# Optimization experiments

Measured on AMD Instinct MI355X. Metric: run time of the kernel, lower is better.

Reference implementation:

```python
import jax, jax.numpy as jnp
import numpy as np

N_NODES = 10000
N_EDGES = 640000
F_IN = 128
HID = 128
N_LAYERS = 3
N_ACT = 4096
NEG_SLOPE = 0.2


def setup_inputs() -> dict:
    key = jax.random.key(0)
    ks = jax.random.split(key, 16)
    s = 0.05
    return {
        "x": jax.random.normal(ks[0], (N_NODES, F_IN), jnp.float32),
        "edge_index": jax.random.randint(ks[1], (2, N_EDGES), 0, N_NODES, jnp.int64),
        "action_src": jax.random.randint(ks[2], (N_ACT,), 0, N_NODES, jnp.int64),
        "action_dst": jax.random.randint(ks[3], (N_ACT,), 0, N_NODES, jnp.int64),
        "action_type": jax.random.randint(ks[4], (N_ACT,), 0, 2, jnp.int32),
        "gat_W": jax.random.normal(ks[5], (N_LAYERS, HID, HID), jnp.float32) * s,
        "gat_asrc": jax.random.normal(ks[6], (N_LAYERS, HID), jnp.float32) * s,
        "gat_adst": jax.random.normal(ks[7], (N_LAYERS, HID), jnp.float32) * s,
        "gat_b": jax.random.normal(ks[8], (N_LAYERS, HID), jnp.float32) * s,
        "mlp_W1": jax.random.normal(ks[9], (2 * HID + 1, HID), jnp.float32) * s,
        "mlp_b1": jax.random.normal(ks[10], (HID,), jnp.float32) * s,
        "mlp_W2": jax.random.normal(ks[11], (HID, 1), jnp.float32) * s,
        "mlp_b2": jax.random.normal(ks[12], (1,), jnp.float32) * s,
    }


def _gat_layer(h, src, dst, W, a_src, a_dst, b, n_nodes):
    # PyG GATConv, heads=1: z = h W; e_ij = leaky_relu(a_src.z_j + a_dst.z_i)
    z = h @ W                                   # [N, HID]
    e = jax.nn.leaky_relu((z @ a_src)[src] + (z @ a_dst)[dst], NEG_SLOPE)  # [E+N]
    m = jax.ops.segment_max(e, dst, num_segments=n_nodes)
    m = jnp.where(jnp.isfinite(m), m, 0.0)
    ex = jnp.exp(e - m[dst])
    denom = jax.ops.segment_sum(ex, dst, num_segments=n_nodes)
    alpha = ex / denom[dst]                     # softmax over incoming edges
    out = jax.ops.segment_sum(alpha[:, None] * z[src], dst, num_segments=n_nodes)
    return out + b


def reference(x, edge_index, action_src, action_dst, action_type,
              gat_W, gat_asrc, gat_adst, gat_b,
              mlp_W1, mlp_b1, mlp_W2, mlp_b2):
    n = x.shape[0]
    loop = jnp.arange(n, dtype=edge_index.dtype)  # add_self_loops=True
    src = jnp.concatenate([edge_index[0], loop])
    dst = jnp.concatenate([edge_index[1], loop])
    h = x
    for l in range(N_LAYERS):
        h = jax.nn.relu(_gat_layer(h, src, dst, gat_W[l], gat_asrc[l], gat_adst[l], gat_b[l], n))
    # vectorized action scoring: [h[src], h[dst], type_flag] -> MLP -> scalar
    feat = jnp.concatenate(
        [h[action_src], h[action_dst], action_type.astype(h.dtype)[:, None]], axis=-1)
    hidden = jax.nn.relu(feat @ mlp_W1 + mlp_b1)
    scores = (hidden @ mlp_W2 + mlp_b2)[:, 0]   # [N_ACT]
    return scores
```

## Files before the change

kernel.cpp:

```cpp
#include <hip/hip_runtime.h>
#include <hip/hip_bf16.h>
#include <hip/hip_fp16.h>

#define N_NODES 10000
#define N_EDGES 640000
#define TOT_E   (N_EDGES + N_NODES)
#define HID     128
#define NEG_SLOPE 0.2f
#define N_ACT   4096

#define NBKT   250
#define NPB    40
#define P1_EPB 4096
#define P1_EPT 16
#define P1_BLOCKS 159
#define SLOTP  56

__global__ __launch_bounds__(256) void part1_k(const int* __restrict__ ei,
                                               unsigned* __restrict__ bpart,
                                               int* __restrict__ bcnt) {
    __shared__ int hist[256];
    __shared__ int lofs[256];
    __shared__ int sc[256];
    __shared__ unsigned stage[P1_EPB];
    __shared__ unsigned char bkt_of[P1_EPB];
    int t = threadIdx.x;
    hist[t] = 0;
    __syncthreads();

    unsigned pk[P1_EPT];
    int bk[P1_EPT];
    int e0 = blockIdx.x * P1_EPB;
#pragma unroll
    for (int i = 0; i < P1_EPT; i++) {
        int e = e0 + i * 256 + t;
        if (e < TOT_E) {
            int src, dst;
            if (e < N_EDGES) { src = ei[e]; dst = ei[N_EDGES + e]; }
            else             { src = e - N_EDGES; dst = src; }
            pk[i] = ((unsigned)dst << 16) | (unsigned)src;
            bk[i] = dst / NPB;
            atomicAdd(&hist[bk[i]], 1);
        } else bk[i] = -1;
    }
    __syncthreads();
    int v = hist[t];
    sc[t] = v;
    __syncthreads();
    for (int o = 1; o < 256; o <<= 1) {
        int u = (t >= o) ? sc[t - o] : 0;
        __syncthreads();
        sc[t] += u;
        __syncthreads();
    }
    lofs[t] = sc[t] - v;
    bcnt[blockIdx.x * 256 + t] = v;
    hist[t] = 0;
    __syncthreads();
#pragma unroll
    for (int i = 0; i < P1_EPT; i++) {
        if (bk[i] >= 0) {
            int p = atomicAdd(&hist[bk[i]], 1);
            int slot = lofs[bk[i]] + p;
            stage[slot] = pk[i];
            bkt_of[slot] = (unsigned char)bk[i];
        }
    }
    __syncthreads();
    int nv = min(P1_EPB, TOT_E - e0);
    for (int s = t; s < nv; s += 256) {
        int b = bkt_of[s];
        bpart[b * (P1_BLOCKS * SLOTP) + blockIdx.x * SLOTP + (s - lofs[b])] = stage[s];
    }
}

__global__ __launch_bounds__(256) void part2_k(const unsigned* __restrict__ bpart,
                                               const int* __restrict__ bcnt,
                                               int* __restrict__ csr,
                                               int* __restrict__ offs) {
    __shared__ unsigned ebuf[4096];
    __shared__ int sc[256];
    __shared__ int nhist[NPB];
    __shared__ int bstart_s, cnt_s;
    int b = blockIdx.x, t = threadIdx.x;

    int tot = 0;
    if (t < NBKT)
        for (int blk = 0; blk < P1_BLOCKS; blk++) tot += bcnt[blk * 256 + t];
    sc[t] = (t < NBKT) ? tot : 0;
    __syncthreads();
    for (int o = 1; o < 256; o <<= 1) {
        int u = (t >= o) ? sc[t - o] : 0;
        __syncthreads();
        sc[t] += u;
        __syncthreads();
    }
    if (t == b) { bstart_s = sc[t] - tot; cnt_s = tot; }
    if (b == 0 && t == 255) offs[N_NODES] = sc[255];
    __syncthreads();

    int L = (t < P1_BLOCKS) ? bcnt[t * 256 + b] : 0;
    sc[t] = L;
    __syncthreads();
    for (int o = 1; o < 256; o <<= 1) {
        int u = (t >= o) ? sc[t - o] : 0;
        __syncthreads();
        sc[t] += u;
        __syncthreads();
    }
    int P = sc[t] - L;
    if (t < NPB) nhist[t] = 0;
    if (t < P1_BLOCKS && L > 0) {
        const unsigned* myrun = bpart + b * (P1_BLOCKS * SLOTP) + t * SLOTP;
        for (int i = 0; i < L; i++) ebuf[P + i] = myrun[i];
    }
    __syncthreads();

    int cnt = cnt_s;
    int n0 = b * NPB;
    for (int i = t; i < cnt; i += 256) atomicAdd(&nhist[(ebuf[i] >> 16) - n0], 1);
    __syncthreads();
    if (t < 64) {
        int v2 = (t < NPB) ? nhist[t] : 0;
        int s2 = v2;
        for (int o = 1; o < 64; o <<= 1) {
            int u = __shfl_up(s2, o, 64);
            if (t >= o) s2 += u;
        }
        if (t < NPB) {
            int ofs = bstart_s + s2 - v2;
            nhist[t] = ofs;
            offs[n0 + t] = ofs;
        }
    }
    __syncthreads();
    for (int i = t; i < cnt; i += 256) {
        unsigned pk = ebuf[i];
        int p = atomicAdd(&nhist[(pk >> 16) - n0], 1);
        csr[p] = pk & 0xFFFF;
    }
}

__device__ __forceinline__ void agg_node(const __half2* __restrict__ z2,
                                         const float* __restrict__ zsi, float zdn,
                                         const int* __restrict__ csr, int o0, int deg,
                                         int lane, float& accx, float& accy, float& denom) {
    for (int base = 0; base < deg; base += 64) {
        int j = base + lane;
        int sreg = 0;
        float ex = 0.f;
        if (j < deg) {
            int s = csr[o0 + j];
            sreg = s;
            float e = zsi[s] + zdn;
            e = e > 0.f ? e : NEG_SLOPE * e;
            ex = __expf(e);
        }
        int cnt = min(64, deg - base);
        int q = 0;
        for (; q + 8 <= cnt; q += 8) {
#pragma unroll
            for (int u = 0; u < 8; u++) {
                int sq = __builtin_amdgcn_readlane(sreg, q + u);
                float exq = __uint_as_float(
                    __builtin_amdgcn_readlane(__float_as_uint(ex), q + u));
                denom += exq;
                float2 vf = __half22float2(z2[sq * 64]);
                accx = fmaf(exq, vf.x, accx);
                accy = fmaf(exq, vf.y, accy);
            }
        }
        for (; q < cnt; q++) {
            int sq = __builtin_amdgcn_readlane(sreg, q);
            float exq = __uint_as_float(
                __builtin_amdgcn_readlane(__float_as_uint(ex), q));
            denom += exq;
            float2 vf = __half22float2(z2[sq * 64]);
            accx = fmaf(exq, vf.x, accx);
            accy = fmaf(exq, vf.y, accy);
        }
    }
}

__device__ __forceinline__ void gload_lds16(const float* g, float* l) {
    __builtin_amdgcn_global_load_lds(
        (const __attribute__((address_space(1))) void*)g,
        (__attribute__((address_space(3))) void*)l, 16, 0, 0);
}

__global__ __launch_bounds__(256) void gemm_k(const float* __restrict__ A,
                                              const float* __restrict__ W,
                                              const float* __restrict__ avs,
                                              const float* __restrict__ avd,
                                              __half* __restrict__ z16,
                                              float* __restrict__ zs,
                                              float* __restrict__ zd) {
    __shared__ float As[32 * HID];
    __shared__ float Ws[HID * HID];
    int t = threadIdx.x;
    int w = t >> 6, lane = t & 63;
    int row0 = blockIdx.x * 32;

#pragma unroll
    for (int i = 0; i < 4; i++) {
        int chunk = w * 4 + i;
        long foff = (long)row0 * HID + chunk * 256;
        const float* g = ((foff + 256) <= (long)N_NODES * HID) ? (A + foff + lane * 4)
                                                               : (A + lane * 4);
        gload_lds16(g, As + chunk * 256);
    }
#pragma unroll
    for (int i = 0; i < 16; i++) {
        int chunk = w * 16 + i;
        gload_lds16(W + chunk * 256 + lane * 4, Ws + chunk * 256);
    }
    __syncthreads();

    int tx = t & 31, ty = t >> 5;
    int r0 = ty * 4;
    float acc[4][4] = {{0.f}};
#pragma unroll 4
    for (int k4 = 0; k4 < 32; k4++) {
        float ak[4][4];
#pragma unroll
        for (int r = 0; r < 4; r++) {
            float4 a4 = *(const float4*)&As[(r0 + r) * HID + k4 * 4];
            ak[r][0] = a4.x; ak[r][1] = a4.y; ak[r][2] = a4.z; ak[r][3] = a4.w;
        }
        const float* Wb = &Ws[k4 * 4 * HID + tx * 4];
#pragma unroll
        for (int kk = 0; kk < 4; kk++) {
            float4 wv = *(const float4*)&Wb[kk * HID];
#pragma unroll
            for (int r = 0; r < 4; r++) {
                acc[r][0] = fmaf(ak[r][kk], wv.x, acc[r][0]);
                acc[r][1] = fmaf(ak[r][kk], wv.y, acc[r][1]);
                acc[r][2] = fmaf(ak[r][kk], wv.z, acc[r][2]);
                acc[r][3] = fmaf(ak[r][kk], wv.w, acc[r][3]);
            }
        }
    }
    float4 asv = *(const float4*)&avs[tx * 4];
    float4 adv = *(const float4*)&avd[tx * 4];
#pragma unroll
    for (int r = 0; r < 4; r++) {
        int row = row0 + r0 + r;
        if (row < N_NODES) {
            *(__half2*)&z16[row * HID + tx * 4]     = __floats2half2_rn(acc[r][0], acc[r][1]);
            *(__half2*)&z16[row * HID + tx * 4 + 2] = __floats2half2_rn(acc[r][2], acc[r][3]);
        }
        float ps = acc[r][0] * asv.x + acc[r][1] * asv.y + acc[r][2] * asv.z + acc[r][3] * asv.w;
        float pd = acc[r][0] * adv.x + acc[r][1] * adv.y + acc[r][2] * adv.z + acc[r][3] * adv.w;
#pragma unroll
        for (int o = 1; o < 32; o <<= 1) {
            ps += __shfl_xor(ps, o, 64);
            pd += __shfl_xor(pd, o, 64);
        }
        if (tx == 0 && row < N_NODES) { zs[row] = ps; zd[row] = pd; }
    }
}


__global__ __launch_bounds__(256) void fuse_k(const __half* __restrict__ z16i,
                                              const float* __restrict__ zsi,
                                              const float* __restrict__ zdi,
                                              const int* __restrict__ offs,
                                              const int* __restrict__ csr,
                                              const float* __restrict__ bprev,
                                              const float* __restrict__ W,
                                              const float* __restrict__ avs,
                                              const float* __restrict__ avd,
                                              __half* __restrict__ z16o,
                                              float* __restrict__ zso,
                                              float* __restrict__ zdo) {
    __shared__ float hT[16][HID];
    __shared__ float Wc[2][32 * HID];
    int t = threadIdx.x;
    int w = t >> 6, lane = t & 63;
    int n0 = blockIdx.x * 16;
    float4 wreg[4];
    {
        const float4* Wg = (const float4*)W;
#pragma unroll
        for (int i = 0; i < 4; i++) wreg[i] = Wg[t + 256 * i];
    }
    const __half2* z2 = (const __half2*)z16i + lane;

    float2 bv = *(const float2*)&bprev[2 * lane];
#pragma unroll
    for (int i = 0; i < 4; i++) {
        int ln = w * 4 + i;
        int n = n0 + ln;
        int o0 = offs[n];
        int deg = offs[n + 1] - o0;
        float zdn = zdi[n];
        float accx = 0.f, accy = 0.f, denom = 0.f;
        agg_node(z2, zsi, zdn, csr, o0, deg, lane, accx, accy, denom);
        float inv = 1.0f / denom;
        float vx = accx * inv + bv.x;
        float vy = accy * inv + bv.y;
        float2 hv;
        hv.x = vx > 0.f ? vx : 0.f;
        hv.y = vy > 0.f ? vy : 0.f;
        *(float2*)&hT[ln][2 * lane] = hv;
    }

    int tx = t & 31, ty = t >> 5;
    int r0 = ty * 2, r1 = ty * 2 + 1;
    float acc[2][4] = {{0.f}};
    for (int c = 0; c < 4; c++) {
        float4* dstb = (float4*)Wc[c & 1];
#pragma unroll
        for (int i = 0; i < 4; i++) dstb[t + 256 * i] = wreg[i];
        __syncthreads();
        if (c + 1 < 4) {
            const float4* Wg = (const float4*)(W + (c + 1) * 32 * HID);
#pragma unroll
            for (int i = 0; i < 4; i++) wreg[i] = Wg[t + 256 * i];
        }
        const float* Wb = Wc[c & 1];
        const float* h0 = &hT[r0][c * 32];
        const float* h1 = &hT[r1][c * 32];
#pragma unroll 8
        for (int kk = 0; kk < 32; kk++) {
            float f0 = h0[kk], f1 = h1[kk];
            float4 wv = *(const float4*)&Wb[kk * HID + tx * 4];
            acc[0][0] = fmaf(f0, wv.x, acc[0][0]);
            acc[0][1] = fmaf(f0, wv.y, acc[0][1]);
            acc[0][2] = fmaf(f0, wv.z, acc[0][2]);
            acc[0][3] = fmaf(f0, wv.w, acc[0][3]);
            acc[1][0] = fmaf(f1, wv.x, acc[1][0]);
            acc[1][1] = fmaf(f1, wv.y, acc[1][1]);
            acc[1][2] = fmaf(f1, wv.z, acc[1][2]);
            acc[1][3] = fmaf(f1, wv.w, acc[1][3]);
        }
    }
    float4 asv = *(const float4*)&avs[tx * 4];
    float4 adv = *(const float4*)&avd[tx * 4];
#pragma unroll
    for (int r = 0; r < 2; r++) {
        int row = n0 + (r ? r1 : r0);
        *(__half2*)&z16o[row * HID + tx * 4]     = __floats2half2_rn(acc[r][0], acc[r][1]);
        *(__half2*)&z16o[row * HID + tx * 4 + 2] = __floats2half2_rn(acc[r][2], acc[r][3]);
        float ps = acc[r][0] * asv.x + acc[r][1] * asv.y + acc[r][2] * asv.z + acc[r][3] * asv.w;
        float pd = acc[r][0] * adv.x + acc[r][1] * adv.y + acc[r][2] * adv.z + acc[r][3] * adv.w;
#pragma unroll
        for (int o = 1; o < 32; o <<= 1) {
            ps += __shfl_xor(ps, o, 64);
            pd += __shfl_xor(pd, o, 64);
        }
        if (tx == 0) { zso[row] = ps; zdo[row] = pd; }
    }
}


__global__ __launch_bounds__(256) void agg_k(const __half* __restrict__ z16,
                                             const float* __restrict__ zs,
                                             const float* __restrict__ zd,
                                             const int* __restrict__ offs,
                                             const int* __restrict__ csr,
                                             const float* __restrict__ b,
                                             float* __restrict__ hout) {
    int t = threadIdx.x;
    int w = t >> 6, lane = t & 63;
    int n = blockIdx.x * 4 + w;
    if (n >= N_NODES) return;
    int o0 = offs[n];
    int deg = offs[n + 1] - o0;
    float zdn = zd[n];
    const __half2* z2 = (const __half2*)z16 + lane;
    float accx = 0.f, accy = 0.f, denom = 0.f;
    agg_node(z2, zs, zdn, csr, o0, deg, lane, accx, accy, denom);
    float inv = 1.0f / denom;
    float2 bv = *(const float2*)&b[2 * lane];
    float vx = accx * inv + bv.x;
    float vy = accy * inv + bv.y;
    float2 o;
    o.x = vx > 0.f ? vx : 0.f;
    o.y = vy > 0.f ? vy : 0.f;
    *(float2*)&hout[n * HID + 2 * lane] = o;
}


#define SC_APB 16

__global__ __launch_bounds__(256) void score_k(const float* __restrict__ h,
                                               const int* __restrict__ asrc,
                                               const int* __restrict__ adst,
                                               const int* __restrict__ atype,
                                               const float* __restrict__ W1,
                                               const float* __restrict__ b1,
                                               const float* __restrict__ W2,
                                               const float* __restrict__ b2,
                                               float* __restrict__ out) {
    __shared__ float featT[257][SC_APB + 1];
    __shared__ float Wc[2][32 * HID];
    int t = threadIdx.x;
    int a0 = blockIdx.x * SC_APB;

    float4 wreg[4];
    {
        const float4* Wg = (const float4*)W1;
#pragma unroll
        for (int i = 0; i < 4; i++) wreg[i] = Wg[t + 256 * i];
    }
    for (int idx = t; idx < SC_APB * 128; idx += 256) {
        int a = idx >> 7, c = idx & 127;
        featT[c][a]       = h[asrc[a0 + a] * HID + c];
        featT[128 + c][a] = h[adst[a0 + a] * HID + c];
    }
    if (t < SC_APB) featT[256][t] = (float)atype[a0 + t];

    int cg = t & 31, ap = t >> 5;
    float4 bv = *(const float4*)&b1[cg * 4];
    float acc0[4] = {bv.x, bv.y, bv.z, bv.w};
    float acc1[4] = {bv.x, bv.y, bv.z, bv.w};

    for (int c = 0; c < 8; c++) {
        float4* dstb = (float4*)Wc[c & 1];
#pragma unroll
        for (int i = 0; i < 4; i++) dstb[t + 256 * i] = wreg[i];
        __syncthreads();
        if (c + 1 < 8) {
            const float4* Wg = (const float4*)(W1 + (c + 1) * 32 * HID);
#pragma unroll
            for (int i = 0; i < 4; i++) wreg[i] = Wg[t + 256 * i];
        }
        const float* Wb = Wc[c & 1];
        const float* fT = &featT[c * 32][0];
#pragma unroll 8
        for (int kk = 0; kk < 32; kk++) {
            float4 wv = *(const float4*)&Wb[kk * HID + cg * 4];
            float f0 = fT[kk * (SC_APB + 1) + ap * 2];
            float f1 = fT[kk * (SC_APB + 1) + ap * 2 + 1];
            acc0[0] = fmaf(f0, wv.x, acc0[0]);
            acc0[1] = fmaf(f0, wv.y, acc0[1]);
            acc0[2] = fmaf(f0, wv.z, acc0[2]);
            acc0[3] = fmaf(f0, wv.w, acc0[3]);
            acc1[0] = fmaf(f1, wv.x, acc1[0]);
            acc1[1] = fmaf(f1, wv.y, acc1[1]);
            acc1[2] = fmaf(f1, wv.z, acc1[2]);
            acc1[3] = fmaf(f1, wv.w, acc1[3]);
        }
    }
    {
        float4 wv = *(const float4*)&W1[256 * HID + cg * 4];
        float f0 = featT[256][ap * 2];
        float f1 = featT[256][ap * 2 + 1];
        acc0[0] = fmaf(f0, wv.x, acc0[0]); acc0[1] = fmaf(f0, wv.y, acc0[1]);
        acc0[2] = fmaf(f0, wv.z, acc0[2]); acc0[3] = fmaf(f0, wv.w, acc0[3]);
        acc1[0] = fmaf(f1, wv.x, acc1[0]); acc1[1] = fmaf(f1, wv.y, acc1[1]);
        acc1[2] = fmaf(f1, wv.z, acc1[2]); acc1[3] = fmaf(f1, wv.w, acc1[3]);
    }
    float4 w2v = *(const float4*)&W2[cg * 4];
    float v0 = 0.f, v1 = 0.f;
    v0 += (acc0[0] > 0.f ? acc0[0] : 0.f) * w2v.x;
    v0 += (acc0[1] > 0.f ? acc0[1] : 0.f) * w2v.y;
    v0 += (acc0[2] > 0.f ? acc0[2] : 0.f) * w2v.z;
    v0 += (acc0[3] > 0.f ? acc0[3] : 0.f) * w2v.w;
    v1 += (acc1[0] > 0.f ? acc1[0] : 0.f) * w2v.x;
    v1 += (acc1[1] > 0.f ? acc1[1] : 0.f) * w2v.y;
    v1 += (acc1[2] > 0.f ? acc1[2] : 0.f) * w2v.z;
    v1 += (acc1[3] > 0.f ? acc1[3] : 0.f) * w2v.w;
#pragma unroll
    for (int o = 1; o < 32; o <<= 1) {
        v0 += __shfl_xor(v0, o, 64);
        v1 += __shfl_xor(v1, o, 64);
    }
    if (cg == 0) {
        out[a0 + ap * 2]     = v0 + b2[0];
        out[a0 + ap * 2 + 1] = v1 + b2[0];
    }
}


extern "C" void kernel_launch(void* const* d_in, const int* in_sizes, int n_in,
                              void* d_out, int out_size, void* d_ws, size_t ws_size,
                              hipStream_t stream) {
    const float* x   = (const float*)d_in[0];
    const int* ei    = (const int*)d_in[1];
    const int* asrc  = (const int*)d_in[2];
    const int* adst  = (const int*)d_in[3];
    const int* atype = (const int*)d_in[4];
    const float* gW  = (const float*)d_in[5];
    const float* gas = (const float*)d_in[6];
    const float* gad = (const float*)d_in[7];
    const float* gb  = (const float*)d_in[8];
    const float* W1  = (const float*)d_in[9];
    const float* b1  = (const float*)d_in[10];
    const float* W2  = (const float*)d_in[11];
    const float* b2  = (const float*)d_in[12];
    float* out = (float*)d_out;

    __half* z16A = (__half*)d_ws;
    __half* z16B = z16A + N_NODES * HID;
    float* h3   = (float*)(z16B + N_NODES * HID);
    float* zsA  = h3 + N_NODES * HID;
    float* zdA  = zsA + N_NODES;
    float* zsB  = zdA + N_NODES;
    float* zdB  = zsB + N_NODES;
    int* offs   = (int*)(zdB + N_NODES);
    int* csr    = offs + (N_NODES + 1);
    int* bcnt   = csr + TOT_E;
    unsigned* bpart = (unsigned*)(bcnt + P1_BLOCKS * 256);

    part1_k<<<P1_BLOCKS, 256, 0, stream>>>(ei, bpart, bcnt);
    part2_k<<<NBKT, 256, 0, stream>>>(bpart, bcnt, csr, offs);

    gemm_k<<<(N_NODES + 31) / 32, 256, 0, stream>>>(x, gW, gas, gad, z16A, zsA, zdA);
    fuse_k<<<N_NODES / 16, 256, 0, stream>>>(z16A, zsA, zdA, offs, csr, gb,
                                             gW + 1 * HID * HID, gas + 1 * HID, gad + 1 * HID,
                                             z16B, zsB, zdB);
    fuse_k<<<N_NODES / 16, 256, 0, stream>>>(z16B, zsB, zdB, offs, csr, gb + 1 * HID,
                                             gW + 2 * HID * HID, gas + 2 * HID, gad + 2 * HID,
                                             z16A, zsA, zdA);
    agg_k<<<(N_NODES + 3) / 4, 256, 0, stream>>>(z16A, zsA, zdA, offs, csr,
                                                 gb + 2 * HID, h3);
    score_k<<<N_ACT / SC_APB, 256, 0, stream>>>(h3, asrc, adst, atype,
                                                W1, b1, W2, b2, out);
}
```

Before: 214.1 us.

## Merge CSR build with first GEMM, pipeline gathers, shrink fuse blocks

Merges the CSR second pass (part2_k) and the first-layer GEMM into one launch, with blocks split by blockIdx, so the two independent stages run concurrently and one launch is saved. The CSR pass now sums bucket counts with unrolled accumulators and copies runs wave-cooperatively instead of one thread per run. The aggregation inner loop software-pipelines the half2 gathers so the next 8 neighbour loads are issued before the current 8 are accumulated. fuse_k now handles 8 nodes per block instead of 16, giving twice as many blocks but reloading W in more blocks.

```diff
diff --git a/kernel.cpp b/kernel.cpp
--- a/kernel.cpp
+++ b/kernel.cpp
@@ -15,6 +15,7 @@
 #define P1_EPT 16
 #define P1_BLOCKS 159
 #define SLOTP  56
+#define G_BLOCKS 313
 
 __global__ __launch_bounds__(256) void part1_k(const int* __restrict__ ei,
                                                unsigned* __restrict__ bpart,
@@ -71,73 +72,6 @@
     for (int s = t; s < nv; s += 256) {
         int b = bkt_of[s];
         bpart[b * (P1_BLOCKS * SLOTP) + blockIdx.x * SLOTP + (s - lofs[b])] = stage[s];
-    }
-}
-
-__global__ __launch_bounds__(256) void part2_k(const unsigned* __restrict__ bpart,
-                                               const int* __restrict__ bcnt,
-                                               int* __restrict__ csr,
-                                               int* __restrict__ offs) {
-    __shared__ unsigned ebuf[4096];
-    __shared__ int sc[256];
-    __shared__ int nhist[NPB];
-    __shared__ int bstart_s, cnt_s;
-    int b = blockIdx.x, t = threadIdx.x;
-
-    int tot = 0;
-    if (t < NBKT)
-        for (int blk = 0; blk < P1_BLOCKS; blk++) tot += bcnt[blk * 256 + t];
-    sc[t] = (t < NBKT) ? tot : 0;
-    __syncthreads();
-    for (int o = 1; o < 256; o <<= 1) {
-        int u = (t >= o) ? sc[t - o] : 0;
-        __syncthreads();
-        sc[t] += u;
-        __syncthreads();
-    }
-    if (t == b) { bstart_s = sc[t] - tot; cnt_s = tot; }
-    if (b == 0 && t == 255) offs[N_NODES] = sc[255];
-    __syncthreads();
-
-    int L = (t < P1_BLOCKS) ? bcnt[t * 256 + b] : 0;
-    sc[t] = L;
-    __syncthreads();
-    for (int o = 1; o < 256; o <<= 1) {
-        int u = (t >= o) ? sc[t - o] : 0;
-        __syncthreads();
-        sc[t] += u;
-        __syncthreads();
-    }
-    int P = sc[t] - L;
-    if (t < NPB) nhist[t] = 0;
-    if (t < P1_BLOCKS && L > 0) {
-        const unsigned* myrun = bpart + b * (P1_BLOCKS * SLOTP) + t * SLOTP;
-        for (int i = 0; i < L; i++) ebuf[P + i] = myrun[i];
-    }
-    __syncthreads();
-
-    int cnt = cnt_s;
-    int n0 = b * NPB;
-    for (int i = t; i < cnt; i += 256) atomicAdd(&nhist[(ebuf[i] >> 16) - n0], 1);
-    __syncthreads();
-    if (t < 64) {
-        int v2 = (t < NPB) ? nhist[t] : 0;
-        int s2 = v2;
-        for (int o = 1; o < 64; o <<= 1) {
-            int u = __shfl_up(s2, o, 64);
-            if (t >= o) s2 += u;
-        }
-        if (t < NPB) {
-            int ofs = bstart_s + s2 - v2;
-            nhist[t] = ofs;
-            offs[n0 + t] = ofs;
-        }
-    }
-    __syncthreads();
-    for (int i = t; i < cnt; i += 256) {
-        unsigned pk = ebuf[i];
-        int p = atomicAdd(&nhist[(pk >> 16) - n0], 1);
-        csr[p] = pk & 0xFFFF;
     }
 }
 
@@ -157,18 +91,46 @@
             ex = __expf(e);
         }
         int cnt = min(64, deg - base);
+        int nfull = cnt & ~7;
         int q = 0;
-        for (; q + 8 <= cnt; q += 8) {
+        if (nfull) {
+            __half2 cur[8];
+            float exc[8];
 #pragma unroll
             for (int u = 0; u < 8; u++) {
-                int sq = __builtin_amdgcn_readlane(sreg, q + u);
-                float exq = __uint_as_float(
-                    __builtin_amdgcn_readlane(__float_as_uint(ex), q + u));
-                denom += exq;
-                float2 vf = __half22float2(z2[sq * 64]);
-                accx = fmaf(exq, vf.x, accx);
-                accy = fmaf(exq, vf.y, accy);
-            }
+                int sq = __builtin_amdgcn_readlane(sreg, u);
+                exc[u] = __uint_as_float(
+                    __builtin_amdgcn_readlane(__float_as_uint(ex), u));
+                cur[u] = z2[sq * 64];
+            }
+            for (q = 8; q < nfull; q += 8) {
+                __half2 nxt[8];
+                float exn[8];
+#pragma unroll
+                for (int u = 0; u < 8; u++) {
+                    int sq = __builtin_amdgcn_readlane(sreg, q + u);
+                    exn[u] = __uint_as_float(
+                        __builtin_amdgcn_readlane(__float_as_uint(ex), q + u));
+                    nxt[u] = z2[sq * 64];
+                }
+#pragma unroll
+                for (int u = 0; u < 8; u++) {
+                    denom += exc[u];
+                    float2 vf = __half22float2(cur[u]);
+                    accx = fmaf(exc[u], vf.x, accx);
+                    accy = fmaf(exc[u], vf.y, accy);
+                    cur[u] = nxt[u];
+                    exc[u] = exn[u];
+                }
+            }
+#pragma unroll
+            for (int u = 0; u < 8; u++) {
+                denom += exc[u];
+                float2 vf = __half22float2(cur[u]);
+                accx = fmaf(exc[u], vf.x, accx);
+                accy = fmaf(exc[u], vf.y, accy);
+            }
+            q = nfull;
         }
         for (; q < cnt; q++) {
             int sq = __builtin_amdgcn_readlane(sreg, q);
@@ -188,75 +150,159 @@
         (__attribute__((address_space(3))) void*)l, 16, 0, 0);
 }
 
-__global__ __launch_bounds__(256) void gemm_k(const float* __restrict__ A,
-                                              const float* __restrict__ W,
-                                              const float* __restrict__ avs,
-                                              const float* __restrict__ avd,
-                                              __half* __restrict__ z16,
-                                              float* __restrict__ zs,
-                                              float* __restrict__ zd) {
-    __shared__ float As[32 * HID];
-    __shared__ float Ws[HID * HID];
+__global__ __launch_bounds__(256) void g2_k(const float* __restrict__ A,
+                                            const float* __restrict__ W,
+                                            const float* __restrict__ avs,
+                                            const float* __restrict__ avd,
+                                            __half* __restrict__ z16,
+                                            float* __restrict__ zs,
+                                            float* __restrict__ zd,
+                                            const unsigned* __restrict__ bpart,
+                                            const int* __restrict__ bcnt,
+                                            int* __restrict__ csr,
+                                            int* __restrict__ offs) {
+    __shared__ float smem[20480];
     int t = threadIdx.x;
-    int w = t >> 6, lane = t & 63;
-    int row0 = blockIdx.x * 32;
-
-#pragma unroll
-    for (int i = 0; i < 4; i++) {
-        int chunk = w * 4 + i;
-        long foff = (long)row0 * HID + chunk * 256;
-        const float* g = ((foff + 256) <= (long)N_NODES * HID) ? (A + foff + lane * 4)
-                                                               : (A + lane * 4);
-        gload_lds16(g, As + chunk * 256);
-    }
-#pragma unroll
-    for (int i = 0; i < 16; i++) {
-        int chunk = w * 16 + i;
-        gload_lds16(W + chunk * 256 + lane * 4, Ws + chunk * 256);
-    }
-    __syncthreads();
-
-    int tx = t & 31, ty = t >> 5;
-    int r0 = ty * 4;
-    float acc[4][4] = {{0.f}};
+
+    if (blockIdx.x < G_BLOCKS) {
+        float* As = smem;
+        float* Ws = smem + 32 * HID;
+        int w = t >> 6, lane = t & 63;
+        int row0 = blockIdx.x * 32;
+#pragma unroll
+        for (int i = 0; i < 4; i++) {
+            int chunk = w * 4 + i;
+            long foff = (long)row0 * HID + chunk * 256;
+            const float* g = ((foff + 256) <= (long)N_NODES * HID) ? (A + foff + lane * 4)
+                                                                   : (A + lane * 4);
+            gload_lds16(g, As + chunk * 256);
+        }
+#pragma unroll
+        for (int i = 0; i < 16; i++) {
+            int chunk = w * 16 + i;
+            gload_lds16(W + chunk * 256 + lane * 4, Ws + chunk * 256);
+        }
+        __syncthreads();
+
+        int tx = t & 31, ty = t >> 5;
+        int r0 = ty * 4;
+        float acc[4][4] = {{0.f}};
 #pragma unroll 4
-    for (int k4 = 0; k4 < 32; k4++) {
-        float ak[4][4];
+        for (int k4 = 0; k4 < 32; k4++) {
+            float ak[4][4];
+#pragma unroll
+            for (int r = 0; r < 4; r++) {
+                float4 a4 = *(const float4*)&As[(r0 + r) * HID + k4 * 4];
+                ak[r][0] = a4.x; ak[r][1] = a4.y; ak[r][2] = a4.z; ak[r][3] = a4.w;
+            }
+            const float* Wb = &Ws[k4 * 4 * HID + tx * 4];
+#pragma unroll
+            for (int kk = 0; kk < 4; kk++) {
+                float4 wv = *(const float4*)&Wb[kk * HID];
+#pragma unroll
+                for (int r = 0; r < 4; r++) {
+                    acc[r][0] = fmaf(ak[r][kk], wv.x, acc[r][0]);
+                    acc[r][1] = fmaf(ak[r][kk], wv.y, acc[r][1]);
+                    acc[r][2] = fmaf(ak[r][kk], wv.z, acc[r][2]);
+                    acc[r][3] = fmaf(ak[r][kk], wv.w, acc[r][3]);
+                }
+            }
+        }
+        float4 asv = *(const float4*)&avs[tx * 4];
+        float4 adv = *(const float4*)&avd[tx * 4];
 #pragma unroll
         for (int r = 0; r < 4; r++) {
-            float4 a4 = *(const float4*)&As[(r0 + r) * HID + k4 * 4];
-            ak[r][0] = a4.x; ak[r][1] = a4.y; ak[r][2] = a4.z; ak[r][3] = a4.w;
-        }
-        const float* Wb = &Ws[k4 * 4 * HID + tx * 4];
-#pragma unroll
-        for (int kk = 0; kk < 4; kk++) {
-            float4 wv = *(const float4*)&Wb[kk * HID];
-#pragma unroll
-            for (int r = 0; r < 4; r++) {
-                acc[r][0] = fmaf(ak[r][kk], wv.x, acc[r][0]);
-                acc[r][1] = fmaf(ak[r][kk], wv.y, acc[r][1]);
-                acc[r][2] = fmaf(ak[r][kk], wv.z, acc[r][2]);
-                acc[r][3] = fmaf(ak[r][kk], wv.w, acc[r][3]);
-            }
-        }
-    }
-    float4 asv = *(const float4*)&avs[tx * 4];
-    float4 adv = *(const float4*)&avd[tx * 4];
-#pragma unroll
-    for (int r = 0; r < 4; r++) {
-        int row = row0 + r0 + r;
-        if (row < N_NODES) {
-            *(__half2*)&z16[row * HID + tx * 4]     = __floats2half2_rn(acc[r][0], acc[r][1]);
-            *(__half2*)&z16[row * HID + tx * 4 + 2] = __floats2half2_rn(acc[r][2], acc[r][3]);
-        }
-        float ps = acc[r][0] * asv.x + acc[r][1] * asv.y + acc[r][2] * asv.z + acc[r][3] * asv.w;
-        float pd = acc[r][0] * adv.x + acc[r][1] * adv.y + acc[r][2] * adv.z + acc[r][3] * adv.w;
-#pragma unroll
-        for (int o = 1; o < 32; o <<= 1) {
-            ps += __shfl_xor(ps, o, 64);
-            pd += __shfl_xor(pd, o, 64);
-        }
-        if (tx == 0 && row < N_NODES) { zs[row] = ps; zd[row] = pd; }
+            int row = row0 + r0 + r;
+            if (row < N_NODES) {
+                *(__half2*)&z16[row * HID + tx * 4]     = __floats2half2_rn(acc[r][0], acc[r][1]);
+                *(__half2*)&z16[row * HID + tx * 4 + 2] = __floats2half2_rn(acc[r][2], acc[r][3]);
+            }
+            float ps = acc[r][0] * asv.x + acc[r][1] * asv.y + acc[r][2] * asv.z + acc[r][3] * asv.w;
+            float pd = acc[r][0] * adv.x + acc[r][1] * adv.y + acc[r][2] * adv.z + acc[r][3] * adv.w;
+#pragma unroll
+            for (int o = 1; o < 32; o <<= 1) {
+                ps += __shfl_xor(ps, o, 64);
+                pd += __shfl_xor(pd, o, 64);
+            }
+            if (tx == 0 && row < N_NODES) { zs[row] = ps; zd[row] = pd; }
+        }
+    } else {
+        int b = blockIdx.x - G_BLOCKS;
+        unsigned* ebuf = (unsigned*)smem;
+        int* sc    = (int*)(smem + 4096);
+        int* Ls    = sc + 256;
+        int* nhist = Ls + 256;
+        __shared__ int bstart_s, cnt_s;
+
+        int tot = 0;
+        if (t < NBKT) {
+            int t0 = 0, t1 = 0, t2 = 0, t3 = 0;
+            int blk = 0;
+            for (; blk + 4 <= P1_BLOCKS; blk += 4) {
+                t0 += bcnt[(blk + 0) * 256 + t];
+                t1 += bcnt[(blk + 1) * 256 + t];
+                t2 += bcnt[(blk + 2) * 256 + t];
+                t3 += bcnt[(blk + 3) * 256 + t];
+            }
+            for (; blk < P1_BLOCKS; blk++) t0 += bcnt[blk * 256 + t];
+            tot = t0 + t1 + t2 + t3;
+        }
+        sc[t] = tot;
+        __syncthreads();
+        for (int o = 1; o < 256; o <<= 1) {
+            int u = (t >= o) ? sc[t - o] : 0;
+            __syncthreads();
+            sc[t] += u;
+            __syncthreads();
+        }
+        if (t == b) { bstart_s = sc[t] - tot; cnt_s = tot; }
+        if (b == 0 && t == 255) offs[N_NODES] = sc[255];
+        __syncthreads();
+
+        int L = (t < P1_BLOCKS) ? bcnt[t * 256 + b] : 0;
+        Ls[t] = L;
+        sc[t] = L;
+        __syncthreads();
+        for (int o = 1; o < 256; o <<= 1) {
+            int u = (t >= o) ? sc[t - o] : 0;
+            __syncthreads();
+            sc[t] += u;
+            __syncthreads();
+        }
+        if (t < NPB) nhist[t] = 0;
+        {
+            int wv = t >> 6, lane = t & 63;
+            const unsigned* bbase = bpart + b * (P1_BLOCKS * SLOTP);
+            for (int r = wv; r < P1_BLOCKS; r += 4) {
+                int Lr = Ls[r];
+                if (lane < Lr) ebuf[(sc[r] - Lr) + lane] = bbase[r * SLOTP + lane];
+            }
+        }
+        __syncthreads();
+
+        int cnt = cnt_s;
+        int n0 = b * NPB;
+        for (int i = t; i < cnt; i += 256) atomicAdd(&nhist[(ebuf[i] >> 16) - n0], 1);
+        __syncthreads();
+        if (t < 64) {
+            int v2 = (t < NPB) ? nhist[t] : 0;
+            int s2 = v2;
+            for (int o = 1; o < 64; o <<= 1) {
+                int u = __shfl_up(s2, o, 64);
+                if (t >= o) s2 += u;
+            }
+            if (t < NPB) {
+                int ofs = bstart_s + s2 - v2;
+                nhist[t] = ofs;
+                offs[n0 + t] = ofs;
+            }
+        }
+        __syncthreads();
+        for (int i = t; i < cnt; i += 256) {
+            unsigned pk = ebuf[i];
+            int p = atomicAdd(&nhist[(pk >> 16) - n0], 1);
+            csr[p] = pk & 0xFFFF;
+        }
     }
 }
 
@@ -273,11 +319,11 @@
                                               __half* __restrict__ z16o,
                                               float* __restrict__ zso,
                                               float* __restrict__ zdo) {
-    __shared__ float hT[16][HID];
+    __shared__ float hT[8][HID];
     __shared__ float Wc[2][32 * HID];
     int t = threadIdx.x;
     int w = t >> 6, lane = t & 63;
-    int n0 = blockIdx.x * 16;
+    int n0 = blockIdx.x * 8;
     float4 wreg[4];
     {
         const float4* Wg = (const float4*)W;
@@ -288,8 +334,8 @@
 
     float2 bv = *(const float2*)&bprev[2 * lane];
 #pragma unroll
-    for (int i = 0; i < 4; i++) {
-        int ln = w * 4 + i;
+    for (int i = 0; i < 2; i++) {
+        int ln = w * 2 + i;
         int n = n0 + ln;
         int o0 = offs[n];
         int deg = offs[n + 1] - o0;
@@ -306,8 +352,7 @@
     }
 
     int tx = t & 31, ty = t >> 5;
-    int r0 = ty * 2, r1 = ty * 2 + 1;
-    float acc[2][4] = {{0.f}};
+    float acc[4] = {0.f, 0.f, 0.f, 0.f};
     for (int c = 0; c < 4; c++) {
         float4* dstb = (float4*)Wc[c & 1];
 #pragma unroll
@@ -319,38 +364,30 @@
             for (int i = 0; i < 4; i++) wreg[i] = Wg[t + 256 * i];
         }
         const float* Wb = Wc[c & 1];
-        const float* h0 = &hT[r0][c * 32];
-        const float* h1 = &hT[r1][c * 32];
+        const float* h0 = &hT[ty][c * 32];
 #pragma unroll 8
         for (int kk = 0; kk < 32; kk++) {
-            float f0 = h0[kk], f1 = h1[kk];
+            float f0 = h0[kk];
             float4 wv = *(const float4*)&Wb[kk * HID + tx * 4];
-            acc[0][0] = fmaf(f0, wv.x, acc[0][0]);
-            acc[0][1] = fmaf(f0, wv.y, acc[0][1]);
-            acc[0][2] = fmaf(f0, wv.z, acc[0][2]);
-            acc[0][3] = fmaf(f0, wv.w, acc[0][3]);
-            acc[1][0] = fmaf(f1, wv.x, acc[1][0]);
-            acc[1][1] = fmaf(f1, wv.y, acc[1][1]);
-            acc[1][2] = fmaf(f1, wv.z, acc[1][2]);
-            acc[1][3] = fmaf(f1, wv.w, acc[1][3]);
+            acc[0] = fmaf(f0, wv.x, acc[0]);
+            acc[1] = fmaf(f0, wv.y, acc[1]);
+            acc[2] = fmaf(f0, wv.z, acc[2]);
+            acc[3] = fmaf(f0, wv.w, acc[3]);
         }
     }
     float4 asv = *(const float4*)&avs[tx * 4];
     float4 adv = *(const float4*)&avd[tx * 4];
-#pragma unroll
-    for (int r = 0; r < 2; r++) {
-        int row = n0 + (r ? r1 : r0);
-        *(__half2*)&z16o[row * HID + tx * 4]     = __floats2half2_rn(acc[r][0], acc[r][1]);
-        *(__half2*)&z16o[row * HID + tx * 4 + 2] = __floats2half2_rn(acc[r][2], acc[r][3]);
-        float ps = acc[r][0] * asv.x + acc[r][1] * asv.y + acc[r][2] * asv.z + acc[r][3] * asv.w;
-        float pd = acc[r][0] * adv.x + acc[r][1] * adv.y + acc[r][2] * adv.z + acc[r][3] * adv.w;
-#pragma unroll
-        for (int o = 1; o < 32; o <<= 1) {
-            ps += __shfl_xor(ps, o, 64);
-            pd += __shfl_xor(pd, o, 64);
-        }
-        if (tx == 0) { zso[row] = ps; zdo[row] = pd; }
-    }
+    int row = n0 + ty;
+    *(__half2*)&z16o[row * HID + tx * 4]     = __floats2half2_rn(acc[0], acc[1]);
+    *(__half2*)&z16o[row * HID + tx * 4 + 2] = __floats2half2_rn(acc[2], acc[3]);
+    float ps = acc[0] * asv.x + acc[1] * asv.y + acc[2] * asv.z + acc[3] * asv.w;
+    float pd = acc[0] * adv.x + acc[1] * adv.y + acc[2] * adv.z + acc[3] * adv.w;
+#pragma unroll
+    for (int o = 1; o < 32; o <<= 1) {
+        ps += __shfl_xor(ps, o, 64);
+        pd += __shfl_xor(pd, o, 64);
+    }
+    if (tx == 0) { zso[row] = ps; zdo[row] = pd; }
 }
 
 
@@ -505,15 +542,15 @@
     unsigned* bpart = (unsigned*)(bcnt + P1_BLOCKS * 256);
 
     part1_k<<<P1_BLOCKS, 256, 0, stream>>>(ei, bpart, bcnt);
-    part2_k<<<NBKT, 256, 0, stream>>>(bpart, bcnt, csr, offs);
-
-    gemm_k<<<(N_NODES + 31) / 32, 256, 0, stream>>>(x, gW, gas, gad, z16A, zsA, zdA);
-    fuse_k<<<N_NODES / 16, 256, 0, stream>>>(z16A, zsA, zdA, offs, csr, gb,
-                                             gW + 1 * HID * HID, gas + 1 * HID, gad + 1 * HID,
-                                             z16B, zsB, zdB);
-    fuse_k<<<N_NODES / 16, 256, 0, stream>>>(z16B, zsB, zdB, offs, csr, gb + 1 * HID,
-                                             gW + 2 * HID * HID, gas + 2 * HID, gad + 2 * HID,
-                                             z16A, zsA, zdA);
+    g2_k<<<G_BLOCKS + NBKT, 256, 0, stream>>>(x, gW, gas, gad, z16A, zsA, zdA,
+                                              bpart, bcnt, csr, offs);
+
+    fuse_k<<<N_NODES / 8, 256, 0, stream>>>(z16A, zsA, zdA, offs, csr, gb,
+                                            gW + 1 * HID * HID, gas + 1 * HID, gad + 1 * HID,
+                                            z16B, zsB, zdB);
+    fuse_k<<<N_NODES / 8, 256, 0, stream>>>(z16B, zsB, zdB, offs, csr, gb + 1 * HID,
+                                            gW + 2 * HID * HID, gas + 2 * HID, gad + 2 * HID,
+                                            z16A, zsA, zdA);
     agg_k<<<(N_NODES + 3) / 4, 256, 0, stream>>>(z16A, zsA, zdA, offs, csr,
                                                  gb + 2 * HID, h3);
     score_k<<<N_ACT / SC_APB, 256, 0, stream>>>(h3, asrc, adst, atype,
```

Result: no change. 217.6 us (+1.7%).
